# Performance work log

Hardware: AMD Instinct MI355X
Metric: run time of the kernel (lower is better)

Reference implementation:

```python
import jax, jax.numpy as jnp
import numpy as np

B, NA, LD, AD = 2048, 8, 256, 256
D = LD + AD            # token_dim = 512
E, K, H = 4, 2, 8      # n_experts, top_k, n_attention_heads
FFN, HEAD, BINS = 2048, 512, 101
DH = D // H
LN_EPS = 1e-5


def setup_inputs() -> dict:
    key = jax.random.key(0)
    ks = jax.random.split(key, 9)
    s = 0.02
    return {
        "latents": jax.random.normal(ks[0], (B, NA, LD), jnp.float32),
        "actions": jax.random.normal(ks[1], (B, NA, AD), jnp.float32),
        "gate_W": jax.random.normal(ks[2], (NA * D, E), jnp.float32) * s,
        "Wqkv": jax.random.normal(ks[3], (E, D, 3 * D), jnp.float32) * s,
        "bqkv": jnp.zeros((E, 3 * D), jnp.float32),
        "Wo": jax.random.normal(ks[4], (E, D, D), jnp.float32) * s,
        "bo": jnp.zeros((E, D), jnp.float32),
        "ln1_g": jnp.ones((E, D), jnp.float32),
        "ln1_b": jnp.zeros((E, D), jnp.float32),
        "Wf1": jax.random.normal(ks[5], (E, D, FFN), jnp.float32) * s,
        "bf1": jnp.zeros((E, FFN), jnp.float32),
        "Wf2": jax.random.normal(ks[6], (E, FFN, D), jnp.float32) * s,
        "bf2": jnp.zeros((E, D), jnp.float32),
        "ln2_g": jnp.ones((E, D), jnp.float32),
        "ln2_b": jnp.zeros((E, D), jnp.float32),
        "head_W1": jax.random.normal(ks[7], (NA * D, HEAD), jnp.float32) * s,
        "head_b1": jnp.zeros((HEAD,), jnp.float32),
        "head_W2": jax.random.normal(ks[8], (HEAD, BINS), jnp.float32) * s,
        "head_b2": jnp.zeros((BINS,), jnp.float32),
    }


def _layernorm(x, g, b):
    mu = x.mean(-1, keepdims=True)
    var = ((x - mu) ** 2).mean(-1, keepdims=True)
    return (x - mu) / jnp.sqrt(var + LN_EPS) * g + b


def _expert(tokens, Wqkv, bqkv, Wo, bo, g1, b1, Wf1, bf1, Wf2, bf2, g2, b2):
    # tokens: [B, N, D] -> self-attention + FFN block (pre-residual, post-LN)
    b, n, d = tokens.shape
    qkv = tokens @ Wqkv + bqkv                                  # [B, N, 3D]
    q, k, v = jnp.split(qkv, 3, axis=-1)
    heads = lambda x: x.reshape(b, n, H, DH).transpose(0, 2, 1, 3)  # [B, H, N, dh]
    q, k, v = heads(q), heads(k), heads(v)
    scores = jnp.einsum("bhqd,bhkd->bhqk", q, k) / np.float32(np.sqrt(DH))
    attn = jax.nn.softmax(scores, axis=-1)
    ctx = jnp.einsum("bhqk,bhkd->bhqd", attn, v).transpose(0, 2, 1, 3).reshape(b, n, d)
    x = _layernorm(tokens + ctx @ Wo + bo, g1, b1)
    h = jax.nn.relu(x @ Wf1 + bf1) @ Wf2 + bf2
    return _layernorm(x + h, g2, b2)


def _cv2(x):
    # coefficient of variation squared (unbiased var, matches torch .var())
    x = x.astype(jnp.float32)
    return jnp.var(x, ddof=1) / (jnp.mean(x) ** 2 + 1e-10)


def reference(latents, actions, gate_W, Wqkv, bqkv, Wo, bo, ln1_g, ln1_b,
              Wf1, bf1, Wf2, bf2, ln2_g, ln2_b, head_W1, head_b1, head_W2, head_b2):
    tokens = jnp.concatenate([latents, actions], axis=-1)       # [B, NA, D]
    flat = tokens.reshape(B, -1)
    # --- router (eval mode: clean logits, no noise) ---
    logits = flat @ gate_W                                      # [B, E]
    topv, topi = jax.lax.top_k(logits, min(K + 1, E))
    gk = jax.nn.softmax(topv[:, :K], axis=1)
    gates = jnp.zeros_like(logits).at[jnp.arange(B)[:, None], topi[:, :K]].set(gk)
    # --- experts: run all densely; zero-gate tokens contribute nothing,
    #     identical math to the original masked dispatch/combine ---
    expert_out = jax.vmap(_expert, in_axes=(None,) + (0,) * 12)(
        tokens, Wqkv, bqkv, Wo, bo, ln1_g, ln1_b, Wf1, bf1, Wf2, bf2, ln2_g, ln2_b)  # [E, B, N, D]
    mixed = jnp.einsum("be,ebnd->bnd", gates, expert_out)
    reward_logits = jax.nn.relu(mixed.reshape(B, -1) @ head_W1 + head_b1) @ head_W2 + head_b2
    # --- aux: load balancing loss ---
    load = (gates > 0).sum(0)
    lbl = _cv2(gates.sum(0)) + _cv2(load) + jnp.mean(jax.nn.logsumexp(logits, axis=-1))
    return reward_logits, gates, lbl
```

## Files before the change

### kernel.cpp

```cpp
#include <hip/hip_runtime.h>
#include <stdint.h>

#define NB    2048
#define NAG   8
#define NEXP  4
#define LN_EPS 1e-5f

#define OUT_GATES  (2048*101)
#define OUT_LBL    (OUT_GATES + 2048*4)

typedef __attribute__((ext_vector_type(8))) short short8;
typedef __attribute__((ext_vector_type(4))) float f32x4;

#define MFMA_BF16(a,b,c) __builtin_amdgcn_mfma_f32_16x16x32_bf16((a),(b),(c),0,0,0)

__device__ __forceinline__ float bf2f(unsigned short h){
  union { unsigned int u; float f; } v; v.u = ((unsigned int)h) << 16; return v.f;
}
__device__ __forceinline__ unsigned short f2bf(float x){
  union { float f; unsigned int u; } v; v.f = x;
  unsigned int r = v.u + 0x7FFFu + ((v.u >> 16) & 1u);
  return (unsigned short)(r >> 16);
}
union bfpack8 { short8 v; unsigned short u[8]; };

__device__ __forceinline__ void gload16(const void* g, void* l){
  __builtin_amdgcn_global_load_lds(
      (const __attribute__((address_space(1))) void*)g,
      (__attribute__((address_space(3))) void*)l, 16, 0, 0);
}

#define FBAR() do{ asm volatile("" ::: "memory"); \
                   __builtin_amdgcn_s_barrier(); \
                   asm volatile("" ::: "memory"); }while(0)

#define OFF_WQKVT  0ULL
#define OFF_WOT    6291456ULL
#define OFF_WF1T   8388608ULL
#define OFF_WF2T   16777216ULL
#define OFF_HW1T   25165824ULL
#define OFF_HW2T   29360128ULL
#define OFF_XBF    29474816ULL
#define OFF_SLOTO  63029248ULL
#define OFF_HID    96583680ULL
#define OFF_JOBS   98680832ULL
#define OFF_SLOTW  98713600ULL
#define OFF_LSE    98729984ULL
#define OFF_CNT    98738176ULL
#define WS_NEED    98738192ULL

__global__ __launch_bounds__(256) void k_transpose_cast(const float* __restrict__ src,
    unsigned short* __restrict__ dst, int R, int C){
  __shared__ float tile[32][33];
  int e = blockIdx.z;
  int c0 = blockIdx.x*32, r0 = blockIdx.y*32;
  const float* s = src + (size_t)e*R*C;
  unsigned short* d = dst + (size_t)e*C*R;
  int tx = threadIdx.x & 31, ty = threadIdx.x >> 5;
  for(int yy = ty; yy < 32; yy += 8){
    int r = r0+yy, c = c0+tx;
    if(r<R && c<C) tile[yy][tx] = s[(size_t)r*C + c];
  }
  __syncthreads();
  for(int yy = ty; yy < 32; yy += 8){
    int oc = c0+yy, orr = r0+tx;
    if(oc<C && orr<R) d[(size_t)oc*R + orr] = f2bf(tile[tx][yy]);
  }
}

__global__ __launch_bounds__(256) void k_router(const float* __restrict__ lat,
    const float* __restrict__ act, const float* __restrict__ gateW,
    float* __restrict__ gates_out, int* __restrict__ jobs, int* __restrict__ cnt,
    float* __restrict__ slot_w, float* __restrict__ lse_arr){
  int b = blockIdx.x, t = threadIdx.x;
  float a0=0.f,a1=0.f,a2=0.f,a3=0.f;
  for(int i=t;i<4096;i+=256){
    int n=i>>9, d=i&511;
    float v = (d<256)? lat[((size_t)b*8+n)*256 + d] : act[((size_t)b*8+n)*256 + (d-256)];
    float4 gw = *(const float4*)&gateW[(size_t)i*4];
    a0 += v*gw.x; a1 += v*gw.y; a2 += v*gw.z; a3 += v*gw.w;
  }
  __shared__ float red[4][256];
  red[0][t]=a0; red[1][t]=a1; red[2][t]=a2; red[3][t]=a3;
  __syncthreads();
  for(int s=128;s>0;s>>=1){
    if(t<s){ red[0][t]+=red[0][t+s]; red[1][t]+=red[1][t+s]; red[2][t]+=red[2][t+s]; red[3][t]+=red[3][t+s]; }
    __syncthreads();
  }
  if(t==0){
    float lg[4] = {red[0][0], red[1][0], red[2][0], red[3][0]};
    int i1=0; for(int e=1;e<4;e++) if(lg[e]>lg[i1]) i1=e;
    int i2=-1; for(int e=0;e<4;e++){ if(e==i1) continue; if(i2<0 || lg[e]>lg[i2]) i2=e; }
    float m = lg[i1];
    float e2 = __expf(lg[i2]-m);
    float inv = 1.f/(1.f+e2);
    float w1 = inv, w2 = e2*inv;
    float g[4]={0.f,0.f,0.f,0.f}; g[i1]=w1; g[i2]=w2;
    gates_out[b*4+0]=g[0]; gates_out[b*4+1]=g[1]; gates_out[b*4+2]=g[2]; gates_out[b*4+3]=g[3];
    float s=0.f; for(int e=0;e<4;e++) s += __expf(lg[e]-m);
    lse_arr[b] = m + __logf(s);
    int p1 = atomicAdd(&cnt[i1],1); jobs[i1*2048+p1] = b*2+0; slot_w[b*2+0] = w1;
    int p2 = atomicAdd(&cnt[i2],1); jobs[i2*2048+p2] = b*2+1; slot_w[b*2+1] = w2;
  }
}

__global__ __launch_bounds__(256) void k_finalize(const float* __restrict__ gates,
    const float* __restrict__ lse_arr, const int* __restrict__ cnt, float* __restrict__ lbl){
  __shared__ float r0[256], r1[256], r2[256], r3[256], rl[256];
  int t = threadIdx.x;
  float g0=0.f,g1=0.f,g2=0.f,g3=0.f,l=0.f;
  for(int b=t;b<2048;b+=256){
    g0+=gates[b*4+0]; g1+=gates[b*4+1]; g2+=gates[b*4+2]; g3+=gates[b*4+3];
    l += lse_arr[b];
  }
  r0[t]=g0;r1[t]=g1;r2[t]=g2;r3[t]=g3;rl[t]=l;
  __syncthreads();
  for(int s=128;s>0;s>>=1){
    if(t<s){ r0[t]+=r0[t+s]; r1[t]+=r1[t+s]; r2[t]+=r2[t+s]; r3[t]+=r3[t+s]; rl[t]+=rl[t+s]; }
    __syncthreads();
  }
  if(t==0){
    float gs[4]={r0[0],r1[0],r2[0],r3[0]};
    float ld[4]={(float)cnt[0],(float)cnt[1],(float)cnt[2],(float)cnt[3]};
    float mu1=(gs[0]+gs[1]+gs[2]+gs[3])*0.25f;
    float v1=0.f; for(int i=0;i<4;i++){float d=gs[i]-mu1; v1+=d*d;} v1 *= (1.f/3.f);
    float mu2=(ld[0]+ld[1]+ld[2]+ld[3])*0.25f;
    float v2=0.f; for(int i=0;i<4;i++){float d=ld[i]-mu2; v2+=d*d;} v2 *= (1.f/3.f);
    lbl[0] = v1/(mu1*mu1+1e-10f) + v2/(mu2*mu2+1e-10f) + rl[0]*(1.f/2048.f);
  }
}

#define AT_LDS 149504

#define STAGE_QKV(hh_, ks_, dst_) do{ \
    _Pragma("unroll") \
    for(int _q=0;_q<3;_q++){ \
      unsigned _L = (unsigned)w*3072u + (unsigned)_q*1024u + (unsigned)lane*16u; \
      int _row = (int)(_L>>7); unsigned _pb = _L & 127u; \
      int _gc = (_row<64)? (hh_)*64+_row : (_row<128)? 512+(hh_)*64+(_row-64) : 1024+(hh_)*64+(_row-128); \
      const char* _g = Wq + (size_t)_gc*1024 + (ks_)*128 + (_pb ^ ((unsigned)(_row&7)<<4)); \
      gload16(_g, (dst_) + ((unsigned)w*3072u + (unsigned)_q*1024u)); \
    } }while(0)

#define STAGE_WO(hg_, s_, dst_) do{ \
    int _nh = (s_)>>2, _k2 = (s_)&3; \
    _Pragma("unroll") \
    for(int _q=0;_q<2;_q++){ \
      unsigned _L = (unsigned)w*2048u + (unsigned)_q*1024u + (unsigned)lane*16u; \
      int _row = (int)(_L>>7); unsigned _pb = _L & 127u; \
      const char* _g = WoP + (size_t)(_nh*128+_row)*1024 + (hg_)*512 + _k2*128 \
                     + (_pb ^ ((unsigned)(_row&7)<<4)); \
      gload16(_g, (dst_) + ((unsigned)w*2048u + (unsigned)_q*1024u)); \
    } }while(0)

__global__ __launch_bounds__(512,2) void k_expert_attn(
    const float* __restrict__ lat, const float* __restrict__ act,
    const unsigned short* __restrict__ Wqkv_t, const float* __restrict__ bqkv,
    const unsigned short* __restrict__ Wo_t,   const float* __restrict__ bo,
    const float* __restrict__ ln1g, const float* __restrict__ ln1b,
    const int* __restrict__ jobs, const int* __restrict__ cnt,
    unsigned short* __restrict__ x_bf){
  extern __shared__ char smem[];
  char* Abase = smem;
  char* CTXb  = smem + 65536;
  char* U     = smem + 98304;
  float* SC   = (float*)(smem + 147456);

  int bid = blockIdx.x;
  int e   = (bid&7)>>1;
  int blk = ((bid>>3)<<1) | (bid&1);
  int ne = cnt[e];
  int base = blk*8;
  if(base >= ne) return;
  int t = threadIdx.x;
  int w = t>>6, lane = t&63, lg = lane>>4, lm = lane&15;
  int mt = w>>1, wb = w&1;
  const int* jb = &jobs[e*2048 + base];

  #pragma unroll
  for(int i=0;i<8;i++){
    int u = i*512 + t; int row = u>>6, ch = u&63; int d0 = ch*8;
    int j = row>>3;
    int slot = (base + j < ne) ? jb[j] : jb[0];
    int b = slot>>1, n = row&7;
    const float* src = (d0<256)? &lat[((size_t)b*8+n)*256 + d0]
                               : &act[((size_t)b*8+n)*256 + (d0-256)];
    float4 f0 = *(const float4*)src; float4 f1 = *(const float4*)(src+4);
    bfpack8 pk;
    pk.u[0]=f2bf(f0.x); pk.u[1]=f2bf(f0.y); pk.u[2]=f2bf(f0.z); pk.u[3]=f2bf(f0.w);
    pk.u[4]=f2bf(f1.x); pk.u[5]=f2bf(f1.y); pk.u[6]=f2bf(f1.z); pk.u[7]=f2bf(f1.w);
    *(short8*)(Abase + (((unsigned)(row*1024 + ch*16)) ^ ((unsigned)(row&7)<<4))) = pk.v;
  }
  asm volatile("s_waitcnt lgkmcnt(0)" ::: "memory");

  const char* Wq  = (const char*)(Wqkv_t + (size_t)e*1536*512);
  const char* WoP = (const char*)(Wo_t   + (size_t)e*512*512);
  unsigned short* QH = (unsigned short*)U;

  f32x4 acc2[4][4];
  #pragma unroll
  for(int a=0;a<4;a++)
    #pragma unroll
    for(int b2=0;b2<4;b2++) acc2[a][b2]=(f32x4){0.f,0.f,0.f,0.f};

  for(int hg=0; hg<2; hg++){
    for(int hh=0; hh<4; hh++){
      int h = hg*4 + hh;
      f32x4 acc1[6];
      #pragma unroll
      for(int i=0;i<6;i++) acc1[i]=(f32x4){0.f,0.f,0.f,0.f};

      STAGE_QKV(h, 0, U);
      #pragma unroll
      for(int ks=0; ks<8; ks++){
        char* nxt = U + (((ks+1)&1) ? 24576u : 0u);
        if(ks<7) STAGE_QKV(h, ks+1, nxt);
        if(ks<7) asm volatile("s_waitcnt vmcnt(3)" ::: "memory");
        else     asm volatile("s_waitcnt vmcnt(0)" ::: "memory");
        FBAR();
        const char* bs = U + ((ks&1) ? 24576u : 0u);
        int arow = mt*16+lm;
        #pragma unroll
        for(int half=0; half<2; half++){
          short8 a = *(const short8*)(Abase + (unsigned)arow*1024u
                       + (((unsigned)(ks*128 + half*64 + lg*16)) ^ ((unsigned)(arow&7)<<4)));
          #pragma unroll
          for(int i=0;i<6;i++){
            int brow = (wb*6+i)*16+lm;
            short8 bb = *(const short8*)(bs + (unsigned)brow*128u
                         + (((unsigned)(half*64+lg*16)) ^ ((unsigned)(brow&7)<<4)));
            acc1[i] = MFMA_BF16(a, bb, acc1[i]);
          }
        }
        FBAR();
      }
      #pragma unroll
      for(int i=0;i<6;i++){
        int L = (wb*6+i)*16 + lm;
        int gc = (L<64)? h*64+L : (L<128)? 512+h*64+(L-64) : 1024+h*64+(L-128);
        float bia = bqkv[e*1536 + gc];
        #pragma unroll
        for(int rr=0;rr<4;rr++){
          int row = mt*16 + lg*4 + rr;
          QH[row*200 + L] = f2bf(acc1[i][rr] + bia);
        }
      }
      __syncthreads();
      {
        int r = t>>3, p = t&7, j = r>>3;
        float s = 0.f;
        #pragma unroll
        for(int dd=0; dd<64; dd+=8){
          bfpack8 qa; qa.v = *(const short8*)&QH[r*200 + dd];
          bfpack8 ka; ka.v = *(const short8*)&QH[(j*8+p)*200 + 64 + dd];
          #pragma unroll
          for(int ii=0;ii<8;ii++) s += bf2f(qa.u[ii])*bf2f(ka.u[ii]);
        }
        SC[r*8+p] = s * 0.125f;
      }
      __syncthreads();
      {
        int r = t>>3, p = t&7, j = r>>3;
        float sv[8]; float m = -1e30f;
        #pragma unroll
        for(int kk=0;kk<8;kk++){ sv[kk]=SC[r*8+kk]; m = fmaxf(m, sv[kk]); }
        float ssum = 0.f;
        #pragma unroll
        for(int kk=0;kk<8;kk++){ sv[kk]=__expf(sv[kk]-m); ssum += sv[kk]; }
        float inv = 1.f/ssum;
        float o[8] = {0.f,0.f,0.f,0.f,0.f,0.f,0.f,0.f};
        #pragma unroll
        for(int kk=0;kk<8;kk++){
          float pr = sv[kk]*inv;
          bfpack8 va; va.v = *(const short8*)&QH[(j*8+kk)*200 + 128 + p*8];
          #pragma unroll
          for(int ii=0;ii<8;ii++) o[ii] += pr * bf2f(va.u[ii]);
        }
        bfpack8 pk;
        #pragma unroll
        for(int ii=0;ii<8;ii++) pk.u[ii]=f2bf(o[ii]);
        *(short8*)(CTXb + (((unsigned)(r*512 + hh*128 + p*16)) ^ ((unsigned)(r&7)<<4))) = pk.v;
      }
      __syncthreads();
    }

    STAGE_WO(hg, 0, U);
    #pragma unroll
    for(int s=0; s<16; s++){
      int nh = s>>2, k2 = s&3;
      char* nxt = U + (((s+1)&1) ? 16384u : 0u);
      if(s<15) STAGE_WO(hg, s+1, nxt);
      if(s<15) asm volatile("s_waitcnt vmcnt(2)" ::: "memory");
      else     asm volatile("s_waitcnt vmcnt(0)" ::: "memory");
      FBAR();
      const char* bs = U + ((s&1) ? 16384u : 0u);
      int arow = mt*16+lm;
      #pragma unroll
      for(int half=0; half<2; half++){
        short8 a = *(const short8*)(CTXb + (unsigned)arow*512u
                     + (((unsigned)(k2*128 + half*64 + lg*16)) ^ ((unsigned)(arow&7)<<4)));
        #pragma unroll
        for(int i=0;i<4;i++){
          int brow = (wb*4+i)*16+lm;
          short8 bb = *(const short8*)(bs + (unsigned)brow*128u
                       + (((unsigned)(half*64+lg*16)) ^ ((unsigned)(brow&7)<<4)));
          acc2[nh][i] = MFMA_BF16(a, bb, acc2[nh][i]);
        }
      }
      FBAR();
    }
  }

  #pragma unroll
  for(int nh=0; nh<4; nh++)
    #pragma unroll
    for(int i=0;i<4;i++){
      int gcol = nh*128 + (wb*4+i)*16 + lm;
      float bia = bo[e*512 + gcol];
      #pragma unroll
      for(int rr=0;rr<4;rr++){
        int row = mt*16 + lg*4 + rr;
        int j2 = row>>3;
        int slot = (base+j2<ne)? jb[j2] : jb[0];
        int b = slot>>1, n = row&7;
        float tok = (gcol<256)? lat[((size_t)b*8+n)*256 + gcol]
                              : act[((size_t)b*8+n)*256 + gcol - 256];
        *(unsigned short*)(Abase + (((unsigned)(row*1024 + gcol*2)) ^ ((unsigned)(row&7)<<4)))
            = f2bf(acc2[nh][i][rr] + bia + tok);
      }
    }
  __syncthreads();
  {
    int r = t>>3, p = t&7;
    unsigned rsw = ((unsigned)(r&7))<<4;
    bfpack8 xv[8];
    float sum=0.f, sq=0.f;
    #pragma unroll
    for(int j=0;j<8;j++){
      xv[j].v = *(const short8*)(Abase + (((unsigned)(r*1024 + j*128 + p*16)) ^ rsw));
      #pragma unroll
      for(int ii=0;ii<8;ii++){ float f = bf2f(xv[j].u[ii]); sum += f; sq += f*f; }
    }
    sum += __shfl_xor(sum,1); sq += __shfl_xor(sq,1);
    sum += __shfl_xor(sum,2); sq += __shfl_xor(sq,2);
    sum += __shfl_xor(sum,4); sq += __shfl_xor(sq,4);
    float mu = sum*(1.f/512.f);
    float var = sq*(1.f/512.f) - mu*mu;
    float rstd = rsqrtf(var + LN_EPS);
    int j8 = r>>3;
    if(base + j8 < ne){
      int slot = jb[j8]; int n = r&7;
      unsigned short* dst = &x_bf[((size_t)slot*8+n)*512];
      #pragma unroll
      for(int j=0;j<8;j++){
        bfpack8 pk;
        #pragma unroll
        for(int ii=0;ii<8;ii++){
          int gc = j*64 + p*8 + ii;
          float xvv = (bf2f(xv[j].u[ii]) - mu)*rstd*ln1g[e*512+gc] + ln1b[e*512+gc];
          pk.u[ii] = f2bf(xvv);
        }
        *(short8*)&dst[j*64 + p*8] = pk.v;
      }
    }
  }
}

#define E2_LDS 99328
#define E2_HP  264

#define FFN_STAGE_W1(cc, kk, dst) do{ \
    const char* _Wb = W1 + ((size_t)(cc)*256)*1024; \
    unsigned _Lw = (unsigned)w*4096u; \
    _Pragma("unroll") \
    for(int _q=0;_q<4;_q++){ \
      unsigned _L = _Lw + (unsigned)_q*1024u + (unsigned)lane*16u; \
      int _row = (int)(_L>>7); unsigned _pb = _L&127u; \
      const char* _g = _Wb + (size_t)_row*1024 + (kk)*128 + (_pb ^ ((unsigned)(_row&7)<<4)); \
      gload16(_g, (dst) + (_Lw + (unsigned)_q*1024u)); \
    } }while(0)

#define FFN_STAGE_W2(cc, nn, kk, dst) do{ \
    unsigned _Lw = (unsigned)w*4096u; \
    _Pragma("unroll") \
    for(int _q=0;_q<4;_q++){ \
      unsigned _L = _Lw + (unsigned)_q*1024u + (unsigned)lane*16u; \
      int _row = (int)(_L>>7); unsigned _pb = _L&127u; \
      const char* _g = W2 + (size_t)((nn)*256+_row)*4096 + ((cc)*256+(kk)*64)*2 \
                     + (_pb ^ ((unsigned)(_row&7)<<4)); \
      gload16(_g, (dst) + (_Lw + (unsigned)_q*1024u)); \
    } }while(0)

__global__ __launch_bounds__(512,2) void k_expert_ffn(
    const unsigned short* __restrict__ x_bf,
    const unsigned short* __restrict__ Wf1_t, const float* __restrict__ bf1,
    const unsigned short* __restrict__ Wf2_t, const float* __restrict__ bf2v,
    const float* __restrict__ ln2g, const float* __restrict__ ln2b,
    const int* __restrict__ jobs, const int* __restrict__ cnt,
    unsigned short* __restrict__ slot_out){
  extern __shared__ char smem[];
  char* BSB0 = smem;
  char* BSB1 = smem + 32768;
  unsigned short* HC = (unsigned short*)(smem + 65536);
  unsigned short* PL = (unsigned short*)smem;

  int bid = blockIdx.x;
  int e   = (bid&7)>>1;
  int blk = ((bid>>3)<<1) | (bid&1);
  int ne = cnt[e];
  int base = blk*8;
  if(base >= ne) return;
  int t = threadIdx.x;
  int w = t>>6, lane = t&63, lg = lane>>4, lm = lane&15;
  int mg = w>>2, ng = w&3;
  const int* jb = &jobs[e*2048 + base];
  unsigned bswz = ((unsigned)(lm&7))<<4;

  const char* W1 = (const char*)(Wf1_t + (size_t)e*2048*512);
  const char* W2 = (const char*)(Wf2_t + (size_t)e*512*2048);

  const char* xb[2];
  #pragma unroll
  for(int ms=0;ms<2;ms++){
    int row = mg*32 + ms*16 + lm;
    int j = row>>3;
    int slot = (base+j<ne)? jb[j] : jb[0];
    int n = row&7;
    xb[ms] = (const char*)x_bf + (((size_t)slot*8+n)<<10) + (size_t)(lg*16);
  }

  short8 xf[2][2][2];
  #pragma unroll
  for(int ms=0;ms<2;ms++)
    #pragma unroll
    for(int hf=0;hf<2;hf++)
      xf[0][ms][hf] = *(const short8*)(xb[ms] + hf*64);

  f32x4 acc[2][2][4];
  #pragma unroll
  for(int a=0;a<2;a++)
    #pragma unroll
    for(int b=0;b<2;b++)
      #pragma unroll
      for(int c2=0;c2<4;c2++) acc[a][b][c2]=(f32x4){0.f,0.f,0.f,0.f};

  FFN_STAGE_W1(0, 0, BSB0);

  for(int c=0; c<8; c++){
    f32x4 acc1[2][4];
    #pragma unroll
    for(int b=0;b<2;b++)
      #pragma unroll
      for(int c2=0;c2<4;c2++) acc1[b][c2]=(f32x4){0.f,0.f,0.f,0.f};

    #pragma unroll
    for(int ks=0; ks<8; ks++){
      #pragma unroll
      for(int ms=0;ms<2;ms++)
        #pragma unroll
        for(int hf=0;hf<2;hf++)
          xf[(ks+1)&1][ms][hf] = *(const short8*)(xb[ms] + (((ks+1)&7)*128 + hf*64));
      char* nxt = ((ks+1)&1) ? BSB1 : BSB0;
      if(ks<7) FFN_STAGE_W1(c, ks+1, nxt);
      else     FFN_STAGE_W2(c, 0, 0, nxt);
      asm volatile("s_waitcnt vmcnt(8)" ::: "memory");
      FBAR();
      const char* bs = (ks&1) ? BSB1 : BSB0;
      #pragma unroll
      for(int hf=0;hf<2;hf++){
        #pragma unroll
        for(int ns=0;ns<4;ns++){
          unsigned boff = (unsigned)(((ng*4+ns)*16+lm)*128);
          short8 bb = *(const short8*)(bs + boff + (((unsigned)(hf*64+lg*16)) ^ bswz));
          acc1[0][ns] = MFMA_BF16(xf[ks&1][0][hf], bb, acc1[0][ns]);
          acc1[1][ns] = MFMA_BF16(xf[ks&1][1][hf], bb, acc1[1][ns]);
        }
      }
      if(ks==7){
        #pragma unroll
        for(int ms=0;ms<2;ms++)
          #pragma unroll
          for(int ns=0;ns<4;ns++){
            int colL = ng*64 + ns*16 + lm;
            float bia = bf1[e*2048 + c*256 + colL];
            #pragma unroll
            for(int rr=0;rr<4;rr++){
              int row = mg*32 + ms*16 + lg*4 + rr;
              HC[row*E2_HP + colL] = f2bf(fmaxf(acc1[ms][ns][rr] + bia, 0.f));
            }
          }
        asm volatile("s_waitcnt lgkmcnt(0)" ::: "memory");
      }
      FBAR();
    }

    #pragma unroll
    for(int s2=0; s2<8; s2++){
      const int nh = s2>>2, k2 = s2&3;
      char* nxt = ((s2+1)&1) ? BSB1 : BSB0;
      if(s2<7)      FFN_STAGE_W2(c, (s2+1)>>2, (s2+1)&3, nxt);
      else if(c<7)  FFN_STAGE_W1(c+1, 0, nxt);
      if(s2<7){
        asm volatile("s_waitcnt vmcnt(4)" ::: "memory");
      } else {
        if(c<7) asm volatile("s_waitcnt vmcnt(4)" ::: "memory");
        else    asm volatile("s_waitcnt vmcnt(0)" ::: "memory");
      }
      FBAR();
      const char* bs = (s2&1) ? BSB1 : BSB0;
      #pragma unroll
      for(int hf=0;hf<2;hf++){
        short8 ha0 = *(const short8*)&HC[(mg*32 +      lm)*E2_HP + k2*64 + hf*32 + lg*8];
        short8 ha1 = *(const short8*)&HC[(mg*32 + 16 + lm)*E2_HP + k2*64 + hf*32 + lg*8];
        #pragma unroll
        for(int ns=0;ns<4;ns++){
          unsigned boff = (unsigned)(((ng*4+ns)*16+lm)*128);
          short8 bb = *(const short8*)(bs + boff + (((unsigned)(hf*64+lg*16)) ^ bswz));
          acc[nh][0][ns] = MFMA_BF16(ha0, bb, acc[nh][0][ns]);
          acc[nh][1][ns] = MFMA_BF16(ha1, bb, acc[nh][1][ns]);
        }
      }
      FBAR();
    }
  }

  #pragma unroll
  for(int nh=0;nh<2;nh++)
    #pragma unroll
    for(int ms=0;ms<2;ms++)
      #pragma unroll
      for(int ns=0;ns<4;ns++){
        int col = nh*256 + ng*64 + ns*16 + lm;
        float bia = bf2v[e*512+col];
        #pragma unroll
        for(int rr=0;rr<4;rr++){
          int row = mg*32 + ms*16 + lg*4 + rr;
          PL[row*520 + col] = f2bf(acc[nh][ms][ns][rr] + bia);
        }
      }
  __syncthreads();

  {
    int r = t>>3, p = t&7;
    int j8 = r>>3;
    int slot = (base + j8 < ne) ? jb[j8] : jb[0];
    int n = r&7;
    const unsigned short* xg = &x_bf[((size_t)slot*8+n)*512];
    bfpack8 cv[8];
    float sum=0.f, sq=0.f;
    #pragma unroll
    for(int j=0;j<8;j++){
      bfpack8 pa; pa.v = *(const short8*)&PL[r*520 + j*64 + p*8];
      bfpack8 xa; xa.v = *(const short8*)&xg[j*64 + p*8];
      #pragma unroll
      for(int ii=0;ii<8;ii++){
        float f = bf2f(pa.u[ii]) + bf2f(xa.u[ii]);
        cv[j].u[ii] = f2bf(f);
        f = bf2f(cv[j].u[ii]);
        sum += f; sq += f*f;
      }
    }
    sum += __shfl_xor(sum,1); sq += __shfl_xor(sq,1);
    sum += __shfl_xor(sum,2); sq += __shfl_xor(sq,2);
    sum += __shfl_xor(sum,4); sq += __shfl_xor(sq,4);
    float mu = sum*(1.f/512.f);
    float var = sq*(1.f/512.f) - mu*mu;
    float rstd = rsqrtf(var + LN_EPS);
    if(base + j8 < ne){
      unsigned short* dst = &slot_out[((size_t)slot*8+n)*512];
      #pragma unroll
      for(int j=0;j<8;j++){
        bfpack8 pk;
        #pragma unroll
        for(int ii=0;ii<8;ii++){
          int gc = j*64 + p*8 + ii;
          float xv = (bf2f(cv[j].u[ii]) - mu)*rstd*ln2g[e*512+gc] + ln2b[e*512+gc];
          pk.u[ii] = f2bf(xv);
        }
        *(short8*)&dst[j*64 + p*8] = pk.v;
      }
    }
  }
}

__global__ __launch_bounds__(256) void k_combine(const unsigned short* __restrict__ so,
    const float* __restrict__ slotw, unsigned short* __restrict__ mx){
  int gid = blockIdx.x*256 + threadIdx.x;
  int b = gid >> 9, c8 = gid & 511;
  float w0 = slotw[b*2+0], w1 = slotw[b*2+1];
  bfpack8 x0; x0.v = *(const short8*)&so[((size_t)(b*2+0))*4096 + c8*8];
  bfpack8 x1; x1.v = *(const short8*)&so[((size_t)(b*2+1))*4096 + c8*8];
  bfpack8 o;
  #pragma unroll
  for(int j=0;j<8;j++) o.u[j] = f2bf(w0*bf2f(x0.u[j]) + w1*bf2f(x1.u[j]));
  *(short8*)&mx[(size_t)b*4096 + c8*8] = o.v;
}

#define H_SP 72
__global__ __launch_bounds__(256) void k_head1(const unsigned short* __restrict__ mixbf,
    const unsigned short* __restrict__ hW1t, const float* __restrict__ b1,
    unsigned short* __restrict__ hidden){
  __shared__ unsigned short As[64*H_SP], Bs[64*H_SP];
  int n0 = blockIdx.x*64, m0 = blockIdx.y*64;
  int t = threadIdx.x, w = t>>6, lane = t&63, lg = lane>>4, lm = lane&15;
  f32x4 acc[4]; for(int i=0;i<4;i++) acc[i]=(f32x4){0.f,0.f,0.f,0.f};
  for(int ks=0; ks<64; ks++){
    __syncthreads();
    int k0 = ks*64;
    for(int i=0;i<2;i++){
      int u = i*256 + t; int row = u>>3, ch = u&7;
      *(short8*)&As[row*H_SP + ch*8] = *(const short8*)&mixbf[(size_t)(m0+row)*4096 + k0 + ch*8];
    }
    for(int i=0;i<2;i++){
      int u = i*256 + t; int row = u>>3, ch = u&7;
      *(short8*)&Bs[row*H_SP + ch*8] = *(const short8*)&hW1t[(size_t)(n0+row)*4096 + k0 + ch*8];
    }
    __syncthreads();
    for(int half=0; half<2; half++){
      short8 a = *(const short8*)&As[(w*16+lm)*H_SP + half*32 + lg*8];
      for(int i=0;i<4;i++){
        short8 bb = *(const short8*)&Bs[(i*16+lm)*H_SP + half*32 + lg*8];
        acc[i] = MFMA_BF16(a, bb, acc[i]);
      }
    }
  }
  for(int i=0;i<4;i++){
    int gc = n0 + i*16 + lm; float bia = b1[gc];
    for(int rr=0; rr<4; rr++){
      int row = m0 + w*16 + lg*4 + rr;
      hidden[(size_t)row*512 + gc] = f2bf(fmaxf(acc[i][rr] + bia, 0.f));
    }
  }
}

__global__ __launch_bounds__(256) void k_head2(const unsigned short* __restrict__ hidden,
    const unsigned short* __restrict__ hW2t, const float* __restrict__ b2,
    float* __restrict__ out){
  __shared__ unsigned short As[64*H_SP], Bs[112*H_SP];
  int m0 = blockIdx.x*64;
  int t = threadIdx.x, w = t>>6, lane = t&63, lg = lane>>4, lm = lane&15;
  f32x4 acc[7]; for(int i=0;i<7;i++) acc[i]=(f32x4){0.f,0.f,0.f,0.f};
  for(int ks=0; ks<8; ks++){
    __syncthreads();
    int k0 = ks*64;
    for(int i=0;i<2;i++){
      int u = i*256 + t; int row = u>>3, ch = u&7;
      *(short8*)&As[row*H_SP + ch*8] = *(const short8*)&hidden[(size_t)(m0+row)*512 + k0 + ch*8];
    }
    for(int i=0;i<4;i++){
      int u = i*256 + t;
      if(u < 896){
        int row = u>>3, ch = u&7;
        *(short8*)&Bs[row*H_SP + ch*8] = *(const short8*)&hW2t[(size_t)row*512 + k0 + ch*8];
      }
    }
    __syncthreads();
    for(int half=0; half<2; half++){
      short8 a = *(const short8*)&As[(w*16+lm)*H_SP + half*32 + lg*8];
      for(int i=0;i<7;i++){
        short8 bb = *(const short8*)&Bs[(i*16+lm)*H_SP + half*32 + lg*8];
        acc[i] = MFMA_BF16(a, bb, acc[i]);
      }
    }
  }
  for(int i=0;i<7;i++){
    int col = i*16 + lm;
    if(col < 101){
      float bia = b2[col];
      for(int rr=0; rr<4; rr++){
        int row = m0 + w*16 + lg*4 + rr;
        out[(size_t)row*101 + col] = acc[i][rr] + bia;
      }
    }
  }
}

extern "C" void kernel_launch(void* const* d_in, const int* in_sizes, int n_in,
                              void* d_out, int out_size, void* d_ws, size_t ws_size,
                              hipStream_t stream){
  if(ws_size < WS_NEED) return;
  const float* lat  = (const float*)d_in[0];
  const float* act  = (const float*)d_in[1];
  const float* gateW= (const float*)d_in[2];
  const float* Wqkv = (const float*)d_in[3];
  const float* bqkv = (const float*)d_in[4];
  const float* Wo   = (const float*)d_in[5];
  const float* bo   = (const float*)d_in[6];
  const float* ln1g = (const float*)d_in[7];
  const float* ln1b = (const float*)d_in[8];
  const float* Wf1  = (const float*)d_in[9];
  const float* bf1  = (const float*)d_in[10];
  const float* Wf2  = (const float*)d_in[11];
  const float* bf2v = (const float*)d_in[12];
  const float* ln2g = (const float*)d_in[13];
  const float* ln2b = (const float*)d_in[14];
  const float* hW1  = (const float*)d_in[15];
  const float* hb1  = (const float*)d_in[16];
  const float* hW2  = (const float*)d_in[17];
  const float* hb2  = (const float*)d_in[18];
  float* out = (float*)d_out;
  char* ws = (char*)d_ws;

  unsigned short* WQKVT = (unsigned short*)(ws + OFF_WQKVT);
  unsigned short* WOT   = (unsigned short*)(ws + OFF_WOT);
  unsigned short* WF1T  = (unsigned short*)(ws + OFF_WF1T);
  unsigned short* WF2T  = (unsigned short*)(ws + OFF_WF2T);
  unsigned short* HW1T  = (unsigned short*)(ws + OFF_HW1T);
  unsigned short* HW2T  = (unsigned short*)(ws + OFF_HW2T);
  unsigned short* XBF   = (unsigned short*)(ws + OFF_XBF);
  unsigned short* SLOTO = (unsigned short*)(ws + OFF_SLOTO);
  unsigned short* MIXBF = XBF;
  unsigned short* HID = (unsigned short*)(ws + OFF_HID);
  int* JOBS = (int*)(ws + OFF_JOBS);
  float* SLOTW = (float*)(ws + OFF_SLOTW);
  float* LSE = (float*)(ws + OFF_LSE);
  int* CNT = (int*)(ws + OFF_CNT);

  (void)hipFuncSetAttribute((const void*)k_expert_attn,
      hipFuncAttributeMaxDynamicSharedMemorySize, AT_LDS);
  (void)hipFuncSetAttribute((const void*)k_expert_ffn,
      hipFuncAttributeMaxDynamicSharedMemorySize, E2_LDS);

  hipMemsetAsync(CNT, 0, 16, stream);
  hipMemsetAsync(HW2T, 0, 112*512*2, stream);

  k_transpose_cast<<<dim3(48,16,4),256,0,stream>>>(Wqkv, WQKVT, 512, 1536);
  k_transpose_cast<<<dim3(16,16,4),256,0,stream>>>(Wo,   WOT,   512, 512);
  k_transpose_cast<<<dim3(64,16,4),256,0,stream>>>(Wf1,  WF1T,  512, 2048);
  k_transpose_cast<<<dim3(16,64,4),256,0,stream>>>(Wf2,  WF2T,  2048, 512);
  k_transpose_cast<<<dim3(16,128,1),256,0,stream>>>(hW1, HW1T,  4096, 512);
  k_transpose_cast<<<dim3(4,16,1),256,0,stream>>>(hW2,  HW2T,  512, 101);

  k_router<<<2048,256,0,stream>>>(lat, act, gateW, out + OUT_GATES, JOBS, CNT, SLOTW, LSE);
  k_finalize<<<1,256,0,stream>>>(out + OUT_GATES, LSE, CNT, out + OUT_LBL);

  k_expert_attn<<<1024, 512, AT_LDS, stream>>>(lat, act, WQKVT, bqkv, WOT, bo,
      ln1g, ln1b, JOBS, CNT, XBF);
  k_expert_ffn<<<1024, 512, E2_LDS, stream>>>(XBF, WF1T, bf1, WF2T, bf2v,
      ln2g, ln2b, JOBS, CNT, SLOTO);
  k_combine<<<4096,256,0,stream>>>(SLOTO, SLOTW, MIXBF);

  k_head1<<<dim3(8,32),256,0,stream>>>(MIXBF, HW1T, hb1, HID);
  k_head2<<<32,256,0,stream>>>(HID, HW2T, hb2, out);
}
```

Before: 811.6 us.

## Triple-buffer FFN weight staging to drop trailing barrier per k-step

Replaces the two-buffer LDS ring for W1/W2 tiles in the expert FFN kernel with a three-buffer rotation, and removes the second block barrier in each k-step. With three buffers, the asynchronous load for step i+1 targets the buffer last read at step i-1, which the leading barrier already protects, so the trailing sync becomes unnecessary. A single __syncthreads is added before the epilogue reuses LDS. The cost is a larger LDS footprint (about 132KB per block instead of about 99KB), which could limit how many blocks fit per CU.

New measurement: 780.7 us. 1.04x faster.

```diff
diff --git a/kernel.cpp b/kernel.cpp
--- a/kernel.cpp
+++ b/kernel.cpp
@@ -366,21 +366,20 @@
   }
 }
 
-#define E2_LDS 99328
+#define E2_LDS 132096
 #define E2_HP  264
 
-#define FFN_STAGE_W1(cc, kk, dst) do{ \
-    const char* _Wb = W1 + ((size_t)(cc)*256)*1024; \
+#define FFN_STAGE_W1(cc, kk, dstoff) do{ \
     unsigned _Lw = (unsigned)w*4096u; \
     _Pragma("unroll") \
     for(int _q=0;_q<4;_q++){ \
       unsigned _L = _Lw + (unsigned)_q*1024u + (unsigned)lane*16u; \
       int _row = (int)(_L>>7); unsigned _pb = _L&127u; \
-      const char* _g = _Wb + (size_t)_row*1024 + (kk)*128 + (_pb ^ ((unsigned)(_row&7)<<4)); \
-      gload16(_g, (dst) + (_Lw + (unsigned)_q*1024u)); \
+      const char* _g = W1 + (size_t)((cc)*256+_row)*1024 + (kk)*128 + (_pb ^ ((unsigned)(_row&7)<<4)); \
+      gload16(_g, smem + (dstoff) + _Lw + (unsigned)_q*1024u); \
     } }while(0)
 
-#define FFN_STAGE_W2(cc, nn, kk, dst) do{ \
+#define FFN_STAGE_W2(cc, nn, kk, dstoff) do{ \
     unsigned _Lw = (unsigned)w*4096u; \
     _Pragma("unroll") \
     for(int _q=0;_q<4;_q++){ \
@@ -388,8 +387,10 @@
       int _row = (int)(_L>>7); unsigned _pb = _L&127u; \
       const char* _g = W2 + (size_t)((nn)*256+_row)*4096 + ((cc)*256+(kk)*64)*2 \
                      + (_pb ^ ((unsigned)(_row&7)<<4)); \
-      gload16(_g, (dst) + (_Lw + (unsigned)_q*1024u)); \
+      gload16(_g, smem + (dstoff) + _Lw + (unsigned)_q*1024u); \
     } }while(0)
+
+#define ROT3() do{ unsigned _tmp=cur; cur=nxt; nxt=spr; spr=_tmp; }while(0)
 
 __global__ __launch_bounds__(512,2) void k_expert_ffn(
     const unsigned short* __restrict__ x_bf,
@@ -399,9 +400,7 @@
     const int* __restrict__ jobs, const int* __restrict__ cnt,
     unsigned short* __restrict__ slot_out){
   extern __shared__ char smem[];
-  char* BSB0 = smem;
-  char* BSB1 = smem + 32768;
-  unsigned short* HC = (unsigned short*)(smem + 65536);
+  unsigned short* HC = (unsigned short*)(smem + 98304);
   unsigned short* PL = (unsigned short*)smem;
 
   int bid = blockIdx.x;
@@ -444,7 +443,9 @@
       #pragma unroll
       for(int c2=0;c2<4;c2++) acc[a][b][c2]=(f32x4){0.f,0.f,0.f,0.f};
 
-  FFN_STAGE_W1(0, 0, BSB0);
+  unsigned cur=0u, nxt=32768u, spr=65536u;
+
+  FFN_STAGE_W1(0, 0, cur);
 
   for(int c=0; c<8; c++){
     f32x4 acc1[2][4];
@@ -460,12 +461,11 @@
         #pragma unroll
         for(int hf=0;hf<2;hf++)
           xf[(ks+1)&1][ms][hf] = *(const short8*)(xb[ms] + (((ks+1)&7)*128 + hf*64));
-      char* nxt = ((ks+1)&1) ? BSB1 : BSB0;
       if(ks<7) FFN_STAGE_W1(c, ks+1, nxt);
       else     FFN_STAGE_W2(c, 0, 0, nxt);
       asm volatile("s_waitcnt vmcnt(8)" ::: "memory");
       FBAR();
-      const char* bs = (ks&1) ? BSB1 : BSB0;
+      const char* bs = smem + cur;
       #pragma unroll
       for(int hf=0;hf<2;hf++){
         #pragma unroll
@@ -491,23 +491,18 @@
           }
         asm volatile("s_waitcnt lgkmcnt(0)" ::: "memory");
       }
-      FBAR();
+      ROT3();
     }
 
     #pragma unroll
     for(int s2=0; s2<8; s2++){
       const int nh = s2>>2, k2 = s2&3;
-      char* nxt = ((s2+1)&1) ? BSB1 : BSB0;
       if(s2<7)      FFN_STAGE_W2(c, (s2+1)>>2, (s2+1)&3, nxt);
       else if(c<7)  FFN_STAGE_W1(c+1, 0, nxt);
-      if(s2<7){
-        asm volatile("s_waitcnt vmcnt(4)" ::: "memory");
-      } else {
-        if(c<7) asm volatile("s_waitcnt vmcnt(4)" ::: "memory");
-        else    asm volatile("s_waitcnt vmcnt(0)" ::: "memory");
-      }
+      if(s2==7 && c==7) asm volatile("s_waitcnt vmcnt(0)" ::: "memory");
+      else              asm volatile("s_waitcnt vmcnt(4)" ::: "memory");
       FBAR();
-      const char* bs = (s2&1) ? BSB1 : BSB0;
+      const char* bs = smem + cur;
       #pragma unroll
       for(int hf=0;hf<2;hf++){
         short8 ha0 = *(const short8*)&HC[(mg*32 +      lm)*E2_HP + k2*64 + hf*32 + lg*8];
@@ -520,9 +515,10 @@
           acc[nh][1][ns] = MFMA_BF16(ha1, bb, acc[nh][1][ns]);
         }
       }
-      FBAR();
-    }
-  }
+      ROT3();
+    }
+  }
+  __syncthreads();
 
   #pragma unroll
   for(int nh=0;nh<2;nh++)
```
